# Optimization experiments

Hardware: AMD Instinct MI355X
Metric: run time of the kernel (lower is better)

Reference implementation:

```python
import jax, jax.numpy as jnp
import numpy as np

WIN = 7          # window size
HEADS = 6
HD = 32          # head dim
DISP = WIN // 2  # cyclic shift displacement
DSF = 2          # patch-merging downscaling factor
B, C, H, W = 2, 96, 448, 448
DIM = 192        # hidden_dimension
MLP = 4 * DIM
INNER = HEADS * HD  # 192


def _shift_masks():
    ws, d = WIN, DISP
    ul = np.zeros((ws * ws, ws * ws), np.float32)
    ul[-d * ws:, :-d * ws] = -np.inf
    ul[:-d * ws, -d * ws:] = -np.inf
    lr = np.zeros((ws, ws, ws, ws), np.float32)
    lr[:, -d:, :, :-d] = -np.inf
    lr[:, :-d, :, -d:] = -np.inf
    return jnp.asarray(ul), jnp.asarray(lr.reshape(ws * ws, ws * ws))


def _rel_indices():
    idx = np.array([[i, j] for i in range(WIN) for j in range(WIN)])
    return idx[None, :, :] - idx[:, None, :] + WIN - 1


_UL, _LR = _shift_masks()
_RI = _rel_indices()


def layer_norm(x, g, b, eps=1e-5):
    m = x.mean(-1, keepdims=True)
    v = ((x - m) ** 2).mean(-1, keepdims=True)
    return (x - m) * jax.lax.rsqrt(v + eps) * g + b


def window_attention(x, wqkv, pos, wo, bo, shifted):
    if shifted:
        x = jnp.roll(x, (-DISP, -DISP), (1, 2))
    b, nh, nw, _ = x.shape
    nwh, nww = nh // WIN, nw // WIN
    qkv = x @ wqkv  # [b, nh, nw, 3*INNER], chunk layout (3, heads, hd) along last dim
    t = qkv.reshape(b, nwh, WIN, nww, WIN, 3, HEADS, HD)
    t = t.transpose(5, 0, 6, 1, 3, 2, 4, 7).reshape(3, b, HEADS, nwh * nww, WIN * WIN, HD)
    q, k, v = t[0], t[1], t[2]
    dots = jnp.einsum('bhwid,bhwjd->bhwij', q, k) * (HD ** -0.5)
    dots = dots + pos[_RI[:, :, 0], _RI[:, :, 1]]  # relative position bias [49,49]
    if shifted:
        bias = jnp.zeros((nwh * nww, WIN * WIN, WIN * WIN), dots.dtype)
        bias = bias.at[-nww:].add(_UL)           # bottom row of windows
        bias = bias.at[nww - 1::nww].add(_LR)    # rightmost column of windows
        dots = dots + bias[None, None]
    attn = jax.nn.softmax(dots, axis=-1)
    out = jnp.einsum('bhwij,bhwjd->bhwid', attn, v)
    out = out.reshape(b, HEADS, nwh, nww, WIN, WIN, HD)
    out = out.transpose(0, 2, 4, 3, 5, 1, 6).reshape(b, nh, nw, INNER)
    out = out @ wo + bo
    if shifted:
        out = jnp.roll(out, (DISP, DISP), (1, 2))
    return out


def swin_block(x, ln1g, ln1b, wqkv, pos, wo, bo, ln2g, ln2b, w1, b1, w2, b2, shifted):
    x = x + window_attention(layer_norm(x, ln1g, ln1b), wqkv, pos, wo, bo, shifted)
    h = layer_norm(x, ln2g, ln2b) @ w1 + b1
    h = jax.nn.gelu(h, approximate=False)
    return x + h @ w2 + b2


def setup_inputs() -> dict:
    ks = jax.random.split(jax.random.key(0), 16)
    r = lambda k, shp, s=0.02: jax.random.normal(k, shp, jnp.float32) * s
    inp = {
        'x': jax.random.normal(ks[0], (B, C, H, W), jnp.float32),
        'pm_w': r(ks[1], (C * DSF * DSF, DIM)),
        'pm_b': jnp.zeros((DIM,), jnp.float32),
    }
    i = 2
    for sfx in ('r', 's'):
        inp['ln1g_' + sfx] = jnp.ones((DIM,), jnp.float32)
        inp['ln1b_' + sfx] = jnp.zeros((DIM,), jnp.float32)
        inp['wqkv_' + sfx] = r(ks[i], (DIM, 3 * INNER)); i += 1
        inp['pos_' + sfx] = jax.random.normal(ks[i], (2 * WIN - 1, 2 * WIN - 1), jnp.float32); i += 1
        inp['wo_' + sfx] = r(ks[i], (INNER, DIM)); i += 1
        inp['bo_' + sfx] = jnp.zeros((DIM,), jnp.float32)
        inp['ln2g_' + sfx] = jnp.ones((DIM,), jnp.float32)
        inp['ln2b_' + sfx] = jnp.zeros((DIM,), jnp.float32)
        inp['w1_' + sfx] = r(ks[i], (DIM, MLP)); i += 1
        inp['b1_' + sfx] = jnp.zeros((MLP,), jnp.float32)
        inp['w2_' + sfx] = r(ks[i], (MLP, DIM)); i += 1
        inp['b2_' + sfx] = jnp.zeros((DIM,), jnp.float32)
    return inp


def reference(x, pm_w, pm_b,
              ln1g_r, ln1b_r, wqkv_r, pos_r, wo_r, bo_r, ln2g_r, ln2b_r, w1_r, b1_r, w2_r, b2_r,
              ln1g_s, ln1b_s, wqkv_s, pos_s, wo_s, bo_s, ln2g_s, ln2b_s, w1_s, b1_s, w2_s, b2_s):
    b, c, hh, ww = x.shape
    nh, nw = hh // DSF, ww // DSF
    # PatchMerging: Unfold(k=s=DSF) -> feature layout (c, p1, p2)
    t = x.reshape(b, c, nh, DSF, nw, DSF).transpose(0, 2, 4, 1, 3, 5).reshape(b, nh, nw, c * DSF * DSF)
    t = t @ pm_w + pm_b  # [b, nh, nw, DIM]
    t = swin_block(t, ln1g_r, ln1b_r, wqkv_r, pos_r, wo_r, bo_r, ln2g_r, ln2b_r, w1_r, b1_r, w2_r, b2_r, shifted=False)
    t = swin_block(t, ln1g_s, ln1b_s, wqkv_s, pos_s, wo_s, bo_s, ln2g_s, ln2b_s, w1_s, b1_s, w2_s, b2_s, shifted=True)
    return t.transpose(0, 3, 1, 2)  # [b, DIM, nh, nw]
```

## Files before the change

### kernel.cpp

```cpp
#include <hip/hip_runtime.h>
#include <hip/hip_bf16.h>

#define DISPL 3
#define NHEADS 6
#define HH 224
#define NB 2
#define MROWS (NB*HH*HH)

typedef __attribute__((ext_vector_type(8))) short short8v;
typedef __attribute__((ext_vector_type(4))) float f32x4;

__device__ __forceinline__ float b2f(unsigned short u) {
    unsigned v = ((unsigned)u) << 16;
    return __builtin_bit_cast(float, v);
}
__device__ __forceinline__ unsigned short f2b(float f) {
    unsigned u = __builtin_bit_cast(unsigned, f);
    return (unsigned short)((u + 0x7FFFu + ((u >> 16) & 1u)) >> 16);
}
__device__ __forceinline__ unsigned pack2(float a, float b) {
    return (unsigned)f2b(a) | ((unsigned)f2b(b) << 16);
}

__device__ __forceinline__ short8v regroup(unsigned pa0, unsigned pa1,
                                           unsigned pb0, unsigned pb1,
                                           int iq, int hi) {
    int l0 = iq + 16 * (2 * (hi & 1));
    int l1 = l0 + 16;
    int msel = hi >> 1;
    unsigned a0 = (unsigned)__shfl((int)pa0, l0), a1 = (unsigned)__shfl((int)pa1, l0);
    unsigned b0 = (unsigned)__shfl((int)pb0, l0), b1 = (unsigned)__shfl((int)pb1, l0);
    unsigned c0 = (unsigned)__shfl((int)pa0, l1), c1 = (unsigned)__shfl((int)pa1, l1);
    unsigned d0 = (unsigned)__shfl((int)pb0, l1), d1 = (unsigned)__shfl((int)pb1, l1);
    unsigned r0 = msel ? b0 : a0, r1 = msel ? b1 : a1;
    unsigned r2 = msel ? d0 : c0, r3 = msel ? d1 : c1;
    short8v out;
    ((unsigned*)&out)[0] = r0; ((unsigned*)&out)[1] = r1;
    ((unsigned*)&out)[2] = r2; ((unsigned*)&out)[3] = r3;
    return out;
}

struct WtArgs {
    const float* src[9];
    unsigned short* dst[9];
    int K[9];
    int N[9];
};
__global__ __launch_bounds__(256) void wt9_k(WtArgs a) {
    int seg = blockIdx.y;
    int K = a.K[seg], N = a.N[seg];
    int idx = blockIdx.x * 256 + threadIdx.x;
    if (idx >= K * N) return;
    int n = idx % N, k = idx / N;
    a.dst[seg][(size_t)n * K + k] = f2b(a.src[seg][idx]);
}

__global__ __launch_bounds__(256, 3) void pm_k(const float* __restrict__ x,
                                               const unsigned short* __restrict__ Bt,
                                               const float* __restrict__ bias,
                                               float* __restrict__ tout) {
    __shared__ unsigned short X[64 * 392];
    int t = threadIdx.x, lane = t & 63, w = t >> 6;
    int iq = lane & 15, hi = lane >> 4;
    int m0 = blockIdx.x * 64;
    int lane16 = t & 15, g = t >> 4;
    int base[4];
    #pragma unroll
    for (int rg = 0; rg < 4; rg++) {
        int m = m0 + 16 * rg + lane16;
        int j = m % 224; int bi = m / 224; int i = bi % 224; int b = bi / 224;
        base[rg] = ((b * 96) * 448 + 2 * i) * 448 + 2 * j;
    }
    for (int step = 0; step < 48; step++) {
        int u = g + 16 * step;
        int rg = u & 3, cp = u >> 2;
        int c = cp >> 1, p1 = cp & 1;
        float2 v = *(const float2*)(x + base[rg] + c * 200704 + p1 * 448);
        *(unsigned*)&X[(16 * rg + lane16) * 392 + c * 4 + p1 * 2] = pack2(v.x, v.y);
    }
    __syncthreads();
    f32x4 acc[4][3] = {};
    for (int kk = 0; kk < 12; kk++) {
        short8v a[4], bfr[3];
        #pragma unroll
        for (int mt = 0; mt < 4; mt++)
            a[mt] = *(const short8v*)&X[(16 * mt + iq) * 392 + kk * 32 + hi * 8];
        #pragma unroll
        for (int nt = 0; nt < 3; nt++)
            bfr[nt] = *(const short8v*)&Bt[(size_t)(48 * w + 16 * nt + iq) * 384 + kk * 32 + hi * 8];
        #pragma unroll
        for (int mt = 0; mt < 4; mt++)
            #pragma unroll
            for (int nt = 0; nt < 3; nt++)
                acc[mt][nt] = __builtin_amdgcn_mfma_f32_16x16x32_bf16(a[mt], bfr[nt], acc[mt][nt], 0, 0, 0);
    }
    #pragma unroll
    for (int nt = 0; nt < 3; nt++) {
        int col = 48 * w + 16 * nt + iq;
        float bv = bias[col];
        #pragma unroll
        for (int mt = 0; mt < 4; mt++)
            #pragma unroll
            for (int rr = 0; rr < 4; rr++) {
                size_t row = m0 + 16 * mt + 4 * hi + rr;
                tout[row * 192 + col] = acc[mt][nt][rr] + bv;
            }
    }
}

template<int SHIFT>
__global__ __launch_bounds__(384, 3) void attn_blk_k(
    const unsigned short* __restrict__ wqkvT, const unsigned short* __restrict__ woT,
    const float* __restrict__ ln1g, const float* __restrict__ ln1b,
    const float* __restrict__ pos, const float* __restrict__ bo,
    float* __restrict__ tbuf)
{
    __shared__ unsigned short X[64 * 200];
    __shared__ unsigned short Vt[6][32 * 72];
    __shared__ unsigned short AO[64 * 200];
    __shared__ float Pl[169];
    __shared__ int rtb[64];

    int t = threadIdx.x, lane = t & 63, wid = t >> 6;
    int iq = lane & 15, hi = lane >> 4;
    int window = blockIdx.x;
    int b = window >> 10, wrem = window & 1023;
    int wi = wrem >> 5, wj = wrem & 31;

    auto trow = [&](int p) -> int {
        int pi = p / 7, pj = p - pi * 7;
        int gi = wi * 7 + pi, gj = wj * 7 + pj;
        if (SHIFT) { gi += DISPL; if (gi >= HH) gi -= HH; gj += DISPL; if (gj >= HH) gj -= HH; }
        return (b * HH + gi) * HH + gj;
    };

    if (t < 49) rtb[t] = trow(t);
    for (int q = t; q < 169; q += 384) Pl[q] = pos[q];
    for (int q = t; q < 1500; q += 384) *(unsigned*)&X[49 * 200 + 2 * q] = 0;

    {
        int c8 = t & 7;
        for (int p = t >> 3; p < 49; p += 48) {
            const float* ar = tbuf + (size_t)trow(p) * 192 + c8 * 24;
            float v[24];
            #pragma unroll
            for (int u8 = 0; u8 < 6; u8++) {
                float4 f = *(const float4*)(ar + u8 * 4);
                v[u8 * 4 + 0] = f.x; v[u8 * 4 + 1] = f.y; v[u8 * 4 + 2] = f.z; v[u8 * 4 + 3] = f.w;
            }
            float s = 0.f, sq = 0.f;
            #pragma unroll
            for (int u = 0; u < 24; u++) { s += v[u]; sq += v[u] * v[u]; }
            s += __shfl_xor(s, 1); s += __shfl_xor(s, 2); s += __shfl_xor(s, 4);
            sq += __shfl_xor(sq, 1); sq += __shfl_xor(sq, 2); sq += __shfl_xor(sq, 4);
            float mean = s * (1.f / 192.f);
            float rstd = rsqrtf(sq * (1.f / 192.f) - mean * mean + 1e-5f);
            unsigned short ov[24];
            #pragma unroll
            for (int u8 = 0; u8 < 6; u8++) {
                float4 gg = *(const float4*)(ln1g + c8 * 24 + u8 * 4);
                float4 bb = *(const float4*)(ln1b + c8 * 24 + u8 * 4);
                ov[u8 * 4 + 0] = f2b((v[u8 * 4 + 0] - mean) * rstd * gg.x + bb.x);
                ov[u8 * 4 + 1] = f2b((v[u8 * 4 + 1] - mean) * rstd * gg.y + bb.y);
                ov[u8 * 4 + 2] = f2b((v[u8 * 4 + 2] - mean) * rstd * gg.z + bb.z);
                ov[u8 * 4 + 3] = f2b((v[u8 * 4 + 3] - mean) * rstd * gg.w + bb.w);
            }
            #pragma unroll
            for (int u = 0; u < 3; u++)
                *(short8v*)&X[p * 200 + c8 * 24 + u * 8] = *(short8v*)&ov[u * 8];
        }
    }
    __syncthreads();

    int hq = wid * 32;
    unsigned short* vt = &Vt[wid][0];

    {
        f32x4 dv[2][4] = {};
        for (int kk = 0; kk < 6; kk++) {
            short8v aw[2], bx[4];
            #pragma unroll
            for (int s2 = 0; s2 < 2; s2++)
                aw[s2] = *(const short8v*)&wqkvT[(size_t)(384 + hq + 16 * s2 + iq) * 192 + kk * 32 + hi * 8];
            #pragma unroll
            for (int tg = 0; tg < 4; tg++)
                bx[tg] = *(const short8v*)&X[(16 * tg + iq) * 200 + kk * 32 + hi * 8];
            #pragma unroll
            for (int s2 = 0; s2 < 2; s2++)
                #pragma unroll
                for (int tg = 0; tg < 4; tg++)
                    dv[s2][tg] = __builtin_amdgcn_mfma_f32_16x16x32_bf16(aw[s2], bx[tg], dv[s2][tg], 0, 0, 0);
        }
        #pragma unroll
        for (int s2 = 0; s2 < 2; s2++)
            #pragma unroll
            for (int tg = 0; tg < 4; tg++)
                #pragma unroll
                for (int rr = 0; rr < 4; rr++)
                    vt[(16 * s2 + 4 * hi + rr) * 72 + 16 * tg + iq] = f2b(dv[s2][tg][rr]);
    }

    short8v bQ[4], aK[4];
    {
        f32x4 dq[2][4] = {}, dk[2][4] = {};
        for (int kk = 0; kk < 6; kk++) {
            short8v aq[2], ak[2], bx[4];
            #pragma unroll
            for (int s2 = 0; s2 < 2; s2++) {
                aq[s2] = *(const short8v*)&wqkvT[(size_t)(hq + 16 * s2 + iq) * 192 + kk * 32 + hi * 8];
                ak[s2] = *(const short8v*)&wqkvT[(size_t)(192 + hq + 16 * s2 + iq) * 192 + kk * 32 + hi * 8];
            }
            #pragma unroll
            for (int tg = 0; tg < 4; tg++)
                bx[tg] = *(const short8v*)&X[(16 * tg + iq) * 200 + kk * 32 + hi * 8];
            #pragma unroll
            for (int s2 = 0; s2 < 2; s2++)
                #pragma unroll
                for (int tg = 0; tg < 4; tg++) {
                    dq[s2][tg] = __builtin_amdgcn_mfma_f32_16x16x32_bf16(aq[s2], bx[tg], dq[s2][tg], 0, 0, 0);
                    dk[s2][tg] = __builtin_amdgcn_mfma_f32_16x16x32_bf16(ak[s2], bx[tg], dk[s2][tg], 0, 0, 0);
                }
        }
        #pragma unroll
        for (int tg = 0; tg < 4; tg++) {
            unsigned q00 = pack2(dq[0][tg][0], dq[0][tg][1]), q01 = pack2(dq[0][tg][2], dq[0][tg][3]);
            unsigned q10 = pack2(dq[1][tg][0], dq[1][tg][1]), q11 = pack2(dq[1][tg][2], dq[1][tg][3]);
            bQ[tg] = regroup(q00, q01, q10, q11, iq, hi);
            unsigned k00 = pack2(dk[0][tg][0], dk[0][tg][1]), k01 = pack2(dk[0][tg][2], dk[0][tg][3]);
            unsigned k10 = pack2(dk[1][tg][0], dk[1][tg][1]), k11 = pack2(dk[1][tg][2], dk[1][tg][3]);
            aK[tg] = regroup(k00, k01, k10, k11, iq, hi);
        }
    }

    f32x4 st[4][4] = {};
    #pragma unroll
    for (int jt = 0; jt < 4; jt++)
        #pragma unroll
        for (int it = 0; it < 4; it++)
            st[jt][it] = __builtin_amdgcn_mfma_f32_16x16x32_bf16(aK[jt], bQ[it], st[jt][it], 0, 0, 0);

    const float scale = 0.17677669529663687f;
    unsigned pkp[4][4][2];
    #pragma unroll
    for (int it = 0; it < 4; it++) {
        int i = iq + 16 * it;
        int ic = i > 48 ? 48 : i;
        int ih = ic / 7, iw2 = ic - ih * 7;
        float sv[16];
        #pragma unroll
        for (int jt = 0; jt < 4; jt++) {
            #pragma unroll
            for (int r = 0; r < 4; r++) {
                int jj = 16 * jt + 4 * hi + r;
                float s;
                if (jj < 49) {
                    int jh = jj / 7, jw2 = jj - jh * 7;
                    s = st[jt][it][r] * scale + Pl[(jh - ih + 6) * 13 + (jw2 - iw2 + 6)];
                    if (SHIFT) {
                        bool msk = false;
                        if (wi == 31) msk = msk || ((i >= 28) != (jj >= 28));
                        if (wj == 31) msk = msk || ((iw2 >= 4) != (jw2 >= 4));
                        if (msk) s = -1e30f;
                    }
                } else s = -1e30f;
                sv[jt * 4 + r] = s;
            }
        }
        float mx = sv[0];
        #pragma unroll
        for (int u = 1; u < 16; u++) mx = fmaxf(mx, sv[u]);
        mx = fmaxf(mx, __shfl_xor(mx, 16));
        mx = fmaxf(mx, __shfl_xor(mx, 32));
        float sum = 0.f;
        #pragma unroll
        for (int u = 0; u < 16; u++) { sv[u] = __expf(sv[u] - mx); sum += sv[u]; }
        sum += __shfl_xor(sum, 16);
        sum += __shfl_xor(sum, 32);
        float rinv = 1.0f / sum;
        #pragma unroll
        for (int jt = 0; jt < 4; jt++) {
            pkp[it][jt][0] = pack2(sv[jt * 4 + 0] * rinv, sv[jt * 4 + 1] * rinv);
            pkp[it][jt][1] = pack2(sv[jt * 4 + 2] * rinv, sv[jt * 4 + 3] * rinv);
        }
    }

    f32x4 o[4][2] = {};
    #pragma unroll
    for (int kk = 0; kk < 2; kk++) {
        short8v bV[2];
        #pragma unroll
        for (int ntv = 0; ntv < 2; ntv++)
            bV[ntv] = *(const short8v*)&vt[(iq + 16 * ntv) * 72 + kk * 32 + hi * 8];
        #pragma unroll
        for (int it = 0; it < 4; it++) {
            short8v aP = regroup(pkp[it][2 * kk][0], pkp[it][2 * kk][1],
                                 pkp[it][2 * kk + 1][0], pkp[it][2 * kk + 1][1], iq, hi);
            o[it][0] = __builtin_amdgcn_mfma_f32_16x16x32_bf16(aP, bV[0], o[it][0], 0, 0, 0);
            o[it][1] = __builtin_amdgcn_mfma_f32_16x16x32_bf16(aP, bV[1], o[it][1], 0, 0, 0);
        }
    }
    #pragma unroll
    for (int it = 0; it < 4; it++)
        #pragma unroll
        for (int ntv = 0; ntv < 2; ntv++)
            #pragma unroll
            for (int rr = 0; rr < 4; rr++)
                AO[(16 * it + 4 * hi + rr) * 200 + hq + 16 * ntv + iq] = f2b(o[it][ntv][rr]);
    __syncthreads();

    f32x4 a2[4][2] = {};
    for (int kk = 0; kk < 6; kk++) {
        short8v aA[4], bW[2];
        #pragma unroll
        for (int mt = 0; mt < 4; mt++)
            aA[mt] = *(const short8v*)&AO[(16 * mt + iq) * 200 + kk * 32 + hi * 8];
        #pragma unroll
        for (int nt = 0; nt < 2; nt++)
            bW[nt] = *(const short8v*)&woT[(size_t)(32 * wid + 16 * nt + iq) * 192 + kk * 32 + hi * 8];
        #pragma unroll
        for (int mt = 0; mt < 4; mt++)
            #pragma unroll
            for (int nt = 0; nt < 2; nt++)
                a2[mt][nt] = __builtin_amdgcn_mfma_f32_16x16x32_bf16(aA[mt], bW[nt], a2[mt][nt], 0, 0, 0);
    }
    #pragma unroll
    for (int nt = 0; nt < 2; nt++) {
        int col = 32 * wid + 16 * nt + iq;
        float bv = bo[col];
        #pragma unroll
        for (int mt = 0; mt < 4; mt++)
            #pragma unroll
            for (int rr = 0; rr < 4; rr++) {
                int i = 16 * mt + 4 * hi + rr;
                if (i < 49) {
                    size_t r = (size_t)rtb[i] * 192 + col;
                    tbuf[r] = a2[mt][nt][rr] + bv + tbuf[r];
                }
            }
    }
}

__global__ __launch_bounds__(256, 3) void mlp_k(const unsigned short* __restrict__ w1T,
                                                const unsigned short* __restrict__ w2T,
                                                const float* __restrict__ ln2g,
                                                const float* __restrict__ ln2b,
                                                const float* __restrict__ b1,
                                                const float* __restrict__ b2,
                                                float* __restrict__ tbuf)
{
    __shared__ unsigned short X[64 * 200];
    __shared__ unsigned short Hl[64 * 200];
    int t = threadIdx.x, lane = t & 63, w = t >> 6;
    int iq = lane & 15, hi = lane >> 4;
    int m0 = blockIdx.x * 64;

    {
        int c8 = t & 7, p0 = t >> 3;
        #pragma unroll
        for (int pp = 0; pp < 2; pp++) {
            int p = p0 + 32 * pp;
            const float* ar = tbuf + (size_t)(m0 + p) * 192 + c8 * 24;
            float v[24];
            #pragma unroll
            for (int u8 = 0; u8 < 6; u8++) {
                float4 f = *(const float4*)(ar + u8 * 4);
                v[u8 * 4 + 0] = f.x; v[u8 * 4 + 1] = f.y; v[u8 * 4 + 2] = f.z; v[u8 * 4 + 3] = f.w;
            }
            float s = 0.f, sq = 0.f;
            #pragma unroll
            for (int u = 0; u < 24; u++) { s += v[u]; sq += v[u] * v[u]; }
            s += __shfl_xor(s, 1); s += __shfl_xor(s, 2); s += __shfl_xor(s, 4);
            sq += __shfl_xor(sq, 1); sq += __shfl_xor(sq, 2); sq += __shfl_xor(sq, 4);
            float mean = s * (1.f / 192.f);
            float rstd = rsqrtf(sq * (1.f / 192.f) - mean * mean + 1e-5f);
            unsigned short ov[24];
            #pragma unroll
            for (int u8 = 0; u8 < 6; u8++) {
                float4 gg = *(const float4*)(ln2g + c8 * 24 + u8 * 4);
                float4 bb = *(const float4*)(ln2b + c8 * 24 + u8 * 4);
                ov[u8 * 4 + 0] = f2b((v[u8 * 4 + 0] - mean) * rstd * gg.x + bb.x);
                ov[u8 * 4 + 1] = f2b((v[u8 * 4 + 1] - mean) * rstd * gg.y + bb.y);
                ov[u8 * 4 + 2] = f2b((v[u8 * 4 + 2] - mean) * rstd * gg.z + bb.z);
                ov[u8 * 4 + 3] = f2b((v[u8 * 4 + 3] - mean) * rstd * gg.w + bb.w);
            }
            #pragma unroll
            for (int u = 0; u < 3; u++)
                *(short8v*)&X[p * 200 + c8 * 24 + u * 8] = *(short8v*)&ov[u * 8];
        }
    }
    __syncthreads();

    f32x4 acc2[4][3] = {};
    for (int c = 0; c < 4; c++) {
        f32x4 acc1[4][3] = {};
        for (int kk = 0; kk < 6; kk++) {
            short8v aX[4], bW[3];
            #pragma unroll
            for (int mt = 0; mt < 4; mt++)
                aX[mt] = *(const short8v*)&X[(16 * mt + iq) * 200 + kk * 32 + hi * 8];
            #pragma unroll
            for (int nt = 0; nt < 3; nt++)
                bW[nt] = *(const short8v*)&w1T[(size_t)(c * 192 + 48 * w + 16 * nt + iq) * 192 + kk * 32 + hi * 8];
            #pragma unroll
            for (int mt = 0; mt < 4; mt++)
                #pragma unroll
                for (int nt = 0; nt < 3; nt++)
                    acc1[mt][nt] = __builtin_amdgcn_mfma_f32_16x16x32_bf16(aX[mt], bW[nt], acc1[mt][nt], 0, 0, 0);
        }
        #pragma unroll
        for (int nt = 0; nt < 3; nt++) {
            int col = 48 * w + 16 * nt + iq;
            float bv = b1[c * 192 + col];
            #pragma unroll
            for (int mt = 0; mt < 4; mt++)
                #pragma unroll
                for (int rr = 0; rr < 4; rr++) {
                    float vv = acc1[mt][nt][rr] + bv;
                    vv = 0.5f * vv * (1.0f + erff(vv * 0.70710678118654752f));
                    Hl[(16 * mt + 4 * hi + rr) * 200 + col] = f2b(vv);
                }
        }
        __syncthreads();
        for (int kk = 0; kk < 6; kk++) {
            short8v aH[4], bW[3];
            #pragma unroll
            for (int mt = 0; mt < 4; mt++)
                aH[mt] = *(const short8v*)&Hl[(16 * mt + iq) * 200 + kk * 32 + hi * 8];
            #pragma unroll
            for (int nt = 0; nt < 3; nt++)
                bW[nt] = *(const short8v*)&w2T[(size_t)(48 * w + 16 * nt + iq) * 768 + c * 192 + kk * 32 + hi * 8];
            #pragma unroll
            for (int mt = 0; mt < 4; mt++)
                #pragma unroll
                for (int nt = 0; nt < 3; nt++)
                    acc2[mt][nt] = __builtin_amdgcn_mfma_f32_16x16x32_bf16(aH[mt], bW[nt], acc2[mt][nt], 0, 0, 0);
        }
        __syncthreads();
    }
    #pragma unroll
    for (int nt = 0; nt < 3; nt++) {
        int col = 48 * w + 16 * nt + iq;
        float bv = b2[col];
        #pragma unroll
        for (int mt = 0; mt < 4; mt++)
            #pragma unroll
            for (int rr = 0; rr < 4; rr++) {
                size_t r = (size_t)(m0 + 16 * mt + 4 * hi + rr) * 192 + col;
                tbuf[r] = acc2[mt][nt][rr] + bv + tbuf[r];
            }
    }
}

__global__ __launch_bounds__(256) void tr_k(const float* __restrict__ tin,
                                            float* __restrict__ outp) {
    __shared__ float tile[32][33];
    int bi = blockIdx.x;
    int j0 = blockIdx.y * 32, c0 = blockIdx.z * 32;
    int t = threadIdx.x;
    int tx = t & 31, ty = t >> 5;
    int b = bi / 224, i = bi % 224;
    #pragma unroll
    for (int yy = 0; yy < 32; yy += 8) {
        int j = j0 + ty + yy;
        tile[ty + yy][tx] = tin[((size_t)bi * 224 + j) * 192 + c0 + tx];
    }
    __syncthreads();
    #pragma unroll
    for (int yy = 0; yy < 32; yy += 8) {
        int c = c0 + ty + yy;
        outp[(((size_t)b * 192 + c) * 224 + i) * 224 + j0 + tx] = tile[tx][ty + yy];
    }
}

extern "C" void kernel_launch(void* const* d_in, const int* in_sizes, int n_in,
                              void* d_out, int out_size, void* d_ws, size_t ws_size,
                              hipStream_t stream) {
    (void)in_sizes; (void)n_in; (void)out_size; (void)ws_size;
    const float* x    = (const float*)d_in[0];
    const float* pm_w = (const float*)d_in[1];
    const float* pm_b = (const float*)d_in[2];

    char* ws = (char*)d_ws;
    size_t off = 0;
    float* tbuf = (float*)(ws + off); off += (size_t)MROWS * 192 * 4;
    unsigned short* pm_wt = (unsigned short*)(ws + off); off += 192 * 384 * 2;
    unsigned short* wqkv_t[2]; unsigned short* wo_t[2];
    unsigned short* w1_t[2];   unsigned short* w2_t[2];
    for (int s = 0; s < 2; s++) {
        wqkv_t[s] = (unsigned short*)(ws + off); off += 576 * 192 * 2;
        wo_t[s]   = (unsigned short*)(ws + off); off += 192 * 192 * 2;
        w1_t[s]   = (unsigned short*)(ws + off); off += 768 * 192 * 2;
        w2_t[s]   = (unsigned short*)(ws + off); off += 192 * 768 * 2;
    }

    WtArgs wa;
    wa.src[0] = pm_w; wa.dst[0] = pm_wt; wa.K[0] = 384; wa.N[0] = 192;
    for (int s = 0; s < 2; s++) {
        wa.src[1 + 4 * s] = (const float*)d_in[5 + 12 * s];  wa.dst[1 + 4 * s] = wqkv_t[s]; wa.K[1 + 4 * s] = 192; wa.N[1 + 4 * s] = 576;
        wa.src[2 + 4 * s] = (const float*)d_in[7 + 12 * s];  wa.dst[2 + 4 * s] = wo_t[s];   wa.K[2 + 4 * s] = 192; wa.N[2 + 4 * s] = 192;
        wa.src[3 + 4 * s] = (const float*)d_in[11 + 12 * s]; wa.dst[3 + 4 * s] = w1_t[s];   wa.K[3 + 4 * s] = 192; wa.N[3 + 4 * s] = 768;
        wa.src[4 + 4 * s] = (const float*)d_in[13 + 12 * s]; wa.dst[4 + 4 * s] = w2_t[s];   wa.K[4 + 4 * s] = 768; wa.N[4 + 4 * s] = 192;
    }
    wt9_k<<<dim3(576, 9), 256, 0, stream>>>(wa);

    pm_k<<<MROWS / 64, 256, 0, stream>>>(x, pm_wt, pm_b, tbuf);

    for (int s = 0; s < 2; s++) {
        const float* ln1g = (const float*)d_in[3 + 12 * s];
        const float* ln1b = (const float*)d_in[4 + 12 * s];
        const float* pos  = (const float*)d_in[6 + 12 * s];
        const float* bo   = (const float*)d_in[8 + 12 * s];
        const float* ln2g = (const float*)d_in[9 + 12 * s];
        const float* ln2b = (const float*)d_in[10 + 12 * s];
        const float* b1   = (const float*)d_in[12 + 12 * s];
        const float* b2   = (const float*)d_in[14 + 12 * s];

        if (s == 0) attn_blk_k<0><<<2048, 384, 0, stream>>>(wqkv_t[0], wo_t[0], ln1g, ln1b, pos, bo, tbuf);
        else        attn_blk_k<1><<<2048, 384, 0, stream>>>(wqkv_t[1], wo_t[1], ln1g, ln1b, pos, bo, tbuf);
        mlp_k<<<MROWS / 64, 256, 0, stream>>>(w1_t[s], w2_t[s], ln2g, ln2b, b1, b2, tbuf);
    }

    tr_k<<<dim3(NB * 224, 7, 6), 256, 0, stream>>>(tbuf, (float*)d_out);
}
```

Before: 775.9 us.

## Prefetch MLP weight fragments into registers and use fast tanh GELU

The MLP kernel now loads the W1 and W2 MFMA B-fragments for a whole hidden chunk into registers up front. The next chunk's W1 fragments are prefetched while the W2 GEMM runs, so global load latency overlaps with compute. The erf GELU is replaced with a tanh-form approximation built on __expf, and the chunk and k loops are fully unrolled. The patch-merge GEMM loop also gets a partial unroll. The risk is heavy register pressure under the 3-blocks-per-SM launch bound, which could cause spills or lower occupancy, plus a small numerical change in GELU.

```diff
diff --git a/kernel.cpp b/kernel.cpp
--- a/kernel.cpp
+++ b/kernel.cpp
@@ -20,6 +20,12 @@
 }
 __device__ __forceinline__ unsigned pack2(float a, float b) {
     return (unsigned)f2b(a) | ((unsigned)f2b(b) << 16);
+}
+__device__ __forceinline__ float gelu_f(float x) {
+    float y = 0.7978845608028654f * (x + 0.044715f * x * x * x);
+    float e = __expf(2.0f * y);
+    float th = 1.0f - 2.0f / (1.0f + e);
+    return 0.5f * x * (1.0f + th);
 }
 
 __device__ __forceinline__ short8v regroup(unsigned pa0, unsigned pa1,
@@ -80,6 +86,7 @@
     }
     __syncthreads();
     f32x4 acc[4][3] = {};
+    #pragma unroll 3
     for (int kk = 0; kk < 12; kk++) {
         short8v a[4], bfr[3];
         #pragma unroll
@@ -354,6 +361,9 @@
     int iq = lane & 15, hi = lane >> 4;
     int m0 = blockIdx.x * 64;
 
+    const unsigned short* w1base = w1T + (size_t)(48 * w + iq) * 192 + hi * 8;
+    const unsigned short* w2base = w2T + (size_t)(48 * w + iq) * 768 + hi * 8;
+
     {
         int c8 = t & 7, p0 = t >> 3;
         #pragma unroll
@@ -388,24 +398,37 @@
                 *(short8v*)&X[p * 200 + c8 * 24 + u * 8] = *(short8v*)&ov[u * 8];
         }
     }
+
+    short8v w1f[3][6];
+    #pragma unroll
+    for (int nt = 0; nt < 3; nt++)
+        #pragma unroll
+        for (int kk = 0; kk < 6; kk++)
+            w1f[nt][kk] = *(const short8v*)(w1base + (size_t)(16 * nt) * 192 + kk * 32);
     __syncthreads();
 
     f32x4 acc2[4][3] = {};
+    #pragma unroll
     for (int c = 0; c < 4; c++) {
+        short8v w2f[3][6];
+        #pragma unroll
+        for (int nt = 0; nt < 3; nt++)
+            #pragma unroll
+            for (int kk = 0; kk < 6; kk++)
+                w2f[nt][kk] = *(const short8v*)(w2base + (size_t)(16 * nt) * 768 + c * 192 + kk * 32);
+
         f32x4 acc1[4][3] = {};
+        #pragma unroll
         for (int kk = 0; kk < 6; kk++) {
-            short8v aX[4], bW[3];
+            short8v aX[4];
             #pragma unroll
             for (int mt = 0; mt < 4; mt++)
                 aX[mt] = *(const short8v*)&X[(16 * mt + iq) * 200 + kk * 32 + hi * 8];
             #pragma unroll
-            for (int nt = 0; nt < 3; nt++)
-                bW[nt] = *(const short8v*)&w1T[(size_t)(c * 192 + 48 * w + 16 * nt + iq) * 192 + kk * 32 + hi * 8];
-            #pragma unroll
             for (int mt = 0; mt < 4; mt++)
                 #pragma unroll
                 for (int nt = 0; nt < 3; nt++)
-                    acc1[mt][nt] = __builtin_amdgcn_mfma_f32_16x16x32_bf16(aX[mt], bW[nt], acc1[mt][nt], 0, 0, 0);
+                    acc1[mt][nt] = __builtin_amdgcn_mfma_f32_16x16x32_bf16(aX[mt], w1f[nt][kk], acc1[mt][nt], 0, 0, 0);
         }
         #pragma unroll
         for (int nt = 0; nt < 3; nt++) {
@@ -414,26 +437,30 @@
             #pragma unroll
             for (int mt = 0; mt < 4; mt++)
                 #pragma unroll
-                for (int rr = 0; rr < 4; rr++) {
-                    float vv = acc1[mt][nt][rr] + bv;
-                    vv = 0.5f * vv * (1.0f + erff(vv * 0.70710678118654752f));
-                    Hl[(16 * mt + 4 * hi + rr) * 200 + col] = f2b(vv);
-                }
+                for (int rr = 0; rr < 4; rr++)
+                    Hl[(16 * mt + 4 * hi + rr) * 200 + col] = f2b(gelu_f(acc1[mt][nt][rr] + bv));
         }
         __syncthreads();
+
+        if (c < 3) {
+            #pragma unroll
+            for (int nt = 0; nt < 3; nt++)
+                #pragma unroll
+                for (int kk = 0; kk < 6; kk++)
+                    w1f[nt][kk] = *(const short8v*)(w1base + (size_t)((c + 1) * 192 + 16 * nt) * 192 + kk * 32);
+        }
+
+        #pragma unroll
         for (int kk = 0; kk < 6; kk++) {
-            short8v aH[4], bW[3];
+            short8v aH[4];
             #pragma unroll
             for (int mt = 0; mt < 4; mt++)
                 aH[mt] = *(const short8v*)&Hl[(16 * mt + iq) * 200 + kk * 32 + hi * 8];
             #pragma unroll
-            for (int nt = 0; nt < 3; nt++)
-                bW[nt] = *(const short8v*)&w2T[(size_t)(48 * w + 16 * nt + iq) * 768 + c * 192 + kk * 32 + hi * 8];
-            #pragma unroll
             for (int mt = 0; mt < 4; mt++)
                 #pragma unroll
                 for (int nt = 0; nt < 3; nt++)
-                    acc2[mt][nt] = __builtin_amdgcn_mfma_f32_16x16x32_bf16(aH[mt], bW[nt], acc2[mt][nt], 0, 0, 0);
+                    acc2[mt][nt] = __builtin_amdgcn_mfma_f32_16x16x32_bf16(aH[mt], w2f[nt][kk], acc2[mt][nt], 0, 0, 0);
         }
         __syncthreads();
     }
```

After: 799.4 us. +3.0%, slower.

## Rewrite MLP kernel to keep activations in registers per wave with tanh GELU

Applied to the files above, without the earlier changes.

The MLP kernel now assigns 32 rows to each wave and keeps the layer-normed inputs and the hidden activations in registers. It uses a transposed MFMA formulation and cross-lane regrouping in place of shared-memory staging, which removes the LDS buffers and all block barriers. Exact erf GELU is replaced by a tanh-based approximation computed with exp. Each block now covers 128 rows under a relaxed launch bound, and the patch-merge k-loop gets a partial unroll. The change trades higher register pressure, and with it lower occupancy, plus a small numeric deviation from exact GELU for fewer shared-memory round trips and syncs.

```diff
diff --git a/kernel.cpp b/kernel.cpp
--- a/kernel.cpp
+++ b/kernel.cpp
@@ -20,6 +20,12 @@
 }
 __device__ __forceinline__ unsigned pack2(float a, float b) {
     return (unsigned)f2b(a) | ((unsigned)f2b(b) << 16);
+}
+__device__ __forceinline__ float gelu_f(float x) {
+    float y = 0.7978845608028654f * (x + 0.044715f * x * x * x);
+    float e = __expf(2.0f * y);
+    float th = 1.0f - 2.0f / (1.0f + e);
+    return 0.5f * x * (1.0f + th);
 }
 
 __device__ __forceinline__ short8v regroup(unsigned pa0, unsigned pa1,
@@ -80,6 +86,7 @@
     }
     __syncthreads();
     f32x4 acc[4][3] = {};
+    #pragma unroll 3
     for (int kk = 0; kk < 12; kk++) {
         short8v a[4], bfr[3];
         #pragma unroll
@@ -340,7 +347,7 @@
     }
 }
 
-__global__ __launch_bounds__(256, 3) void mlp_k(const unsigned short* __restrict__ w1T,
+__global__ __launch_bounds__(256, 2) void mlp_k(const unsigned short* __restrict__ w1T,
                                                 const unsigned short* __restrict__ w2T,
                                                 const float* __restrict__ ln2g,
                                                 const float* __restrict__ ln2b,
@@ -348,105 +355,101 @@
                                                 const float* __restrict__ b2,
                                                 float* __restrict__ tbuf)
 {
-    __shared__ unsigned short X[64 * 200];
-    __shared__ unsigned short Hl[64 * 200];
-    int t = threadIdx.x, lane = t & 63, w = t >> 6;
+    int t = threadIdx.x, lane = t & 63, wv = t >> 6;
     int iq = lane & 15, hi = lane >> 4;
-    int m0 = blockIdx.x * 64;
-
-    {
-        int c8 = t & 7, p0 = t >> 3;
-        #pragma unroll
-        for (int pp = 0; pp < 2; pp++) {
-            int p = p0 + 32 * pp;
-            const float* ar = tbuf + (size_t)(m0 + p) * 192 + c8 * 24;
-            float v[24];
-            #pragma unroll
-            for (int u8 = 0; u8 < 6; u8++) {
-                float4 f = *(const float4*)(ar + u8 * 4);
-                v[u8 * 4 + 0] = f.x; v[u8 * 4 + 1] = f.y; v[u8 * 4 + 2] = f.z; v[u8 * 4 + 3] = f.w;
-            }
-            float s = 0.f, sq = 0.f;
-            #pragma unroll
-            for (int u = 0; u < 24; u++) { s += v[u]; sq += v[u] * v[u]; }
-            s += __shfl_xor(s, 1); s += __shfl_xor(s, 2); s += __shfl_xor(s, 4);
-            sq += __shfl_xor(sq, 1); sq += __shfl_xor(sq, 2); sq += __shfl_xor(sq, 4);
-            float mean = s * (1.f / 192.f);
-            float rstd = rsqrtf(sq * (1.f / 192.f) - mean * mean + 1e-5f);
-            unsigned short ov[24];
-            #pragma unroll
-            for (int u8 = 0; u8 < 6; u8++) {
-                float4 gg = *(const float4*)(ln2g + c8 * 24 + u8 * 4);
-                float4 bb = *(const float4*)(ln2b + c8 * 24 + u8 * 4);
-                ov[u8 * 4 + 0] = f2b((v[u8 * 4 + 0] - mean) * rstd * gg.x + bb.x);
-                ov[u8 * 4 + 1] = f2b((v[u8 * 4 + 1] - mean) * rstd * gg.y + bb.y);
-                ov[u8 * 4 + 2] = f2b((v[u8 * 4 + 2] - mean) * rstd * gg.z + bb.z);
-                ov[u8 * 4 + 3] = f2b((v[u8 * 4 + 3] - mean) * rstd * gg.w + bb.w);
-            }
-            #pragma unroll
-            for (int u = 0; u < 3; u++)
-                *(short8v*)&X[p * 200 + c8 * 24 + u * 8] = *(short8v*)&ov[u * 8];
-        }
-    }
-    __syncthreads();
-
-    f32x4 acc2[4][3] = {};
-    for (int c = 0; c < 4; c++) {
-        f32x4 acc1[4][3] = {};
+    int m0 = blockIdx.x * 128 + 32 * wv;
+
+    short8v xf[2][6];
+    #pragma unroll
+    for (int tg = 0; tg < 2; tg++) {
+        int row = m0 + 16 * tg + iq;
+        const float* ar = tbuf + (size_t)row * 192 + hi * 8;
+        float v[6][8];
+        float s = 0.f, sq = 0.f;
+        #pragma unroll
         for (int kk = 0; kk < 6; kk++) {
-            short8v aX[4], bW[3];
-            #pragma unroll
-            for (int mt = 0; mt < 4; mt++)
-                aX[mt] = *(const short8v*)&X[(16 * mt + iq) * 200 + kk * 32 + hi * 8];
-            #pragma unroll
-            for (int nt = 0; nt < 3; nt++)
-                bW[nt] = *(const short8v*)&w1T[(size_t)(c * 192 + 48 * w + 16 * nt + iq) * 192 + kk * 32 + hi * 8];
-            #pragma unroll
-            for (int mt = 0; mt < 4; mt++)
-                #pragma unroll
-                for (int nt = 0; nt < 3; nt++)
-                    acc1[mt][nt] = __builtin_amdgcn_mfma_f32_16x16x32_bf16(aX[mt], bW[nt], acc1[mt][nt], 0, 0, 0);
-        }
-        #pragma unroll
-        for (int nt = 0; nt < 3; nt++) {
-            int col = 48 * w + 16 * nt + iq;
-            float bv = b1[c * 192 + col];
-            #pragma unroll
-            for (int mt = 0; mt < 4; mt++)
-                #pragma unroll
-                for (int rr = 0; rr < 4; rr++) {
-                    float vv = acc1[mt][nt][rr] + bv;
-                    vv = 0.5f * vv * (1.0f + erff(vv * 0.70710678118654752f));
-                    Hl[(16 * mt + 4 * hi + rr) * 200 + col] = f2b(vv);
-                }
-        }
-        __syncthreads();
+            float4 f0 = *(const float4*)(ar + kk * 32);
+            float4 f1 = *(const float4*)(ar + kk * 32 + 4);
+            v[kk][0] = f0.x; v[kk][1] = f0.y; v[kk][2] = f0.z; v[kk][3] = f0.w;
+            v[kk][4] = f1.x; v[kk][5] = f1.y; v[kk][6] = f1.z; v[kk][7] = f1.w;
+            #pragma unroll
+            for (int e = 0; e < 8; e++) { float vv = v[kk][e]; s += vv; sq += vv * vv; }
+        }
+        s  += __shfl_xor(s, 16);  s  += __shfl_xor(s, 32);
+        sq += __shfl_xor(sq, 16); sq += __shfl_xor(sq, 32);
+        float mean = s * (1.f / 192.f);
+        float rstd = rsqrtf(sq * (1.f / 192.f) - mean * mean + 1e-5f);
+        #pragma unroll
         for (int kk = 0; kk < 6; kk++) {
-            short8v aH[4], bW[3];
-            #pragma unroll
-            for (int mt = 0; mt < 4; mt++)
-                aH[mt] = *(const short8v*)&Hl[(16 * mt + iq) * 200 + kk * 32 + hi * 8];
-            #pragma unroll
-            for (int nt = 0; nt < 3; nt++)
-                bW[nt] = *(const short8v*)&w2T[(size_t)(48 * w + 16 * nt + iq) * 768 + c * 192 + kk * 32 + hi * 8];
-            #pragma unroll
-            for (int mt = 0; mt < 4; mt++)
-                #pragma unroll
-                for (int nt = 0; nt < 3; nt++)
-                    acc2[mt][nt] = __builtin_amdgcn_mfma_f32_16x16x32_bf16(aH[mt], bW[nt], acc2[mt][nt], 0, 0, 0);
-        }
-        __syncthreads();
-    }
-    #pragma unroll
-    for (int nt = 0; nt < 3; nt++) {
-        int col = 48 * w + 16 * nt + iq;
+            float4 g0 = *(const float4*)(ln2g + kk * 32 + hi * 8);
+            float4 g1 = *(const float4*)(ln2g + kk * 32 + hi * 8 + 4);
+            float4 b0 = *(const float4*)(ln2b + kk * 32 + hi * 8);
+            float4 b1v = *(const float4*)(ln2b + kk * 32 + hi * 8 + 4);
+            const float gg[8] = {g0.x,g0.y,g0.z,g0.w,g1.x,g1.y,g1.z,g1.w};
+            const float bb[8] = {b0.x,b0.y,b0.z,b0.w,b1v.x,b1v.y,b1v.z,b1v.w};
+            short8v o;
+            #pragma unroll
+            for (int e = 0; e < 8; e++)
+                o[e] = (short)f2b((v[kk][e] - mean) * rstd * gg[e] + bb[e]);
+            xf[tg][kk] = o;
+        }
+    }
+
+    f32x4 acc2[2][12] = {};
+    #pragma unroll 2
+    for (int c = 0; c < 12; c++) {
+        f32x4 a1[2][4] = {};
+        #pragma unroll
+        for (int kk = 0; kk < 6; kk++) {
+            short8v wf[4];
+            #pragma unroll
+            for (int a = 0; a < 4; a++)
+                wf[a] = *(const short8v*)&w1T[(size_t)(c * 64 + 16 * a + iq) * 192 + kk * 32 + hi * 8];
+            #pragma unroll
+            for (int a = 0; a < 4; a++) {
+                a1[0][a] = __builtin_amdgcn_mfma_f32_16x16x32_bf16(wf[a], xf[0][kk], a1[0][a], 0, 0, 0);
+                a1[1][a] = __builtin_amdgcn_mfma_f32_16x16x32_bf16(wf[a], xf[1][kk], a1[1][a], 0, 0, 0);
+            }
+        }
+        unsigned pk[2][4][2];
+        #pragma unroll
+        for (int a = 0; a < 4; a++) {
+            float4 bv = *(const float4*)(b1 + c * 64 + 16 * a + 4 * hi);
+            #pragma unroll
+            for (int tg = 0; tg < 2; tg++) {
+                float g0 = gelu_f(a1[tg][a][0] + bv.x);
+                float g1 = gelu_f(a1[tg][a][1] + bv.y);
+                float g2 = gelu_f(a1[tg][a][2] + bv.z);
+                float g3 = gelu_f(a1[tg][a][3] + bv.w);
+                pk[tg][a][0] = pack2(g0, g1);
+                pk[tg][a][1] = pack2(g2, g3);
+            }
+        }
+        #pragma unroll
+        for (int ks = 0; ks < 2; ks++) {
+            short8v aH0 = regroup(pk[0][2 * ks][0], pk[0][2 * ks][1],
+                                  pk[0][2 * ks + 1][0], pk[0][2 * ks + 1][1], iq, hi);
+            short8v aH1 = regroup(pk[1][2 * ks][0], pk[1][2 * ks][1],
+                                  pk[1][2 * ks + 1][0], pk[1][2 * ks + 1][1], iq, hi);
+            #pragma unroll
+            for (int nt = 0; nt < 12; nt++) {
+                short8v wf2 = *(const short8v*)&w2T[(size_t)(16 * nt + iq) * 768 + c * 64 + ks * 32 + hi * 8];
+                acc2[0][nt] = __builtin_amdgcn_mfma_f32_16x16x32_bf16(aH0, wf2, acc2[0][nt], 0, 0, 0);
+                acc2[1][nt] = __builtin_amdgcn_mfma_f32_16x16x32_bf16(aH1, wf2, acc2[1][nt], 0, 0, 0);
+            }
+        }
+    }
+
+    #pragma unroll
+    for (int nt = 0; nt < 12; nt++) {
+        int col = 16 * nt + iq;
         float bv = b2[col];
         #pragma unroll
-        for (int mt = 0; mt < 4; mt++)
+        for (int tg = 0; tg < 2; tg++)
             #pragma unroll
             for (int rr = 0; rr < 4; rr++) {
-                size_t r = (size_t)(m0 + 16 * mt + 4 * hi + rr) * 192 + col;
-                tbuf[r] = acc2[mt][nt][rr] + bv + tbuf[r];
+                size_t r = (size_t)(m0 + 16 * tg + 4 * hi + rr) * 192 + col;
+                tbuf[r] = acc2[tg][nt][rr] + bv + tbuf[r];
             }
     }
 }
@@ -517,7 +520,7 @@
 
         if (s == 0) attn_blk_k<0><<<2048, 384, 0, stream>>>(wqkv_t[0], wo_t[0], ln1g, ln1b, pos, bo, tbuf);
         else        attn_blk_k<1><<<2048, 384, 0, stream>>>(wqkv_t[1], wo_t[1], ln1g, ln1b, pos, bo, tbuf);
-        mlp_k<<<MROWS / 64, 256, 0, stream>>>(w1_t[s], w2_t[s], ln2g, ln2b, b1, b2, tbuf);
+        mlp_k<<<MROWS / 128, 256, 0, stream>>>(w1_t[s], w2_t[s], ln2g, ln2b, b1, b2, tbuf);
     }
 
     tr_k<<<dim3(NB * 224, 7, 6), 256, 0, stream>>>(tbuf, (float*)d_out);
```

Result: slower. 1.351 ms (+74.1%).
